# Kernel optimization log

Measured on AMD Instinct MI355X. Metric: run time of the kernel, lower is better.

## Reference

```python
import jax, jax.numpy as jnp
import numpy as np
import math

N_HEAD = 16

def setup_inputs() -> dict:
    key = jax.random.key(0)
    ks = jax.random.split(key, 5)
    B, T, C = 4, 2048, 1024
    x = jax.random.normal(ks[0], (B, T, C), dtype=jnp.float32)
    # xavier-uniform-ish scale for dense kernels
    W_attn = jax.random.normal(ks[1], (C, 3 * C), dtype=jnp.float32) * (1.0 / math.sqrt(C))
    b_attn = jnp.zeros((3 * C,), dtype=jnp.float32)
    W_proj = jax.random.normal(ks[2], (C, C), dtype=jnp.float32) * (1.0 / math.sqrt(C))
    b_proj = jnp.zeros((C,), dtype=jnp.float32)
    return {"x": x, "W_attn": W_attn, "b_attn": b_attn, "W_proj": W_proj, "b_proj": b_proj}

def reference(x, W_attn, b_attn, W_proj, b_proj):
    B, T, C = x.shape
    H = N_HEAD
    D = C // H
    qkv = x @ W_attn + b_attn                      # [B,T,3C]
    q, k, v = jnp.split(qkv, 3, axis=-1)
    q = q.reshape(B, T, H, D).transpose(0, 2, 1, 3)  # [B,H,T,D]
    k = k.reshape(B, T, H, D).transpose(0, 2, 1, 3)
    v = v.reshape(B, T, H, D).transpose(0, 2, 1, 3)
    att = jnp.einsum("bhqd,bhkd->bhqk", q, k) * (1.0 / math.sqrt(D))  # [B,H,T,T]
    causal = jnp.tril(jnp.ones((T, T), dtype=bool))
    att = jnp.where(causal, att, jnp.float32(-jnp.inf))
    att = jax.nn.softmax(att, axis=-1)             # exp(att - logsumexp)
    # dropout rates are 0.0 -> identity
    y = jnp.einsum("bhqk,bhkd->bhqd", att, v)      # [B,H,T,D]
    y = y.transpose(0, 2, 1, 3).reshape(B, T, C)
    y = y @ W_proj + b_proj
    return y
```

## Files before the change

### kernel.cpp

```cpp
#include <hip/hip_runtime.h>
#include <hip/hip_bf16.h>

typedef short s16x8 __attribute__((ext_vector_type(8)));
typedef float f32x4 __attribute__((ext_vector_type(4)));
typedef float f32x2 __attribute__((ext_vector_type(2)));

#define MFMA_BF16(A, B, C) __builtin_amdgcn_mfma_f32_16x16x32_bf16(A, B, C, 0, 0, 0)

constexpr int Bn = 4, Tn = 2048, Cn = 1024, Hn = 16, Dn = 64;
constexpr int Mn = Bn * Tn;
constexpr int Nqkv = 3 * Cn;
constexpr float SC = 0.125f * 1.44269504089f;

__device__ __forceinline__ ushort f2bfu(float f) {
    __hip_bfloat16 h = __float2bfloat16(f);
    return *reinterpret_cast<ushort*>(&h);
}
__device__ __forceinline__ uint pkbf(float a, float b) {
    __hip_bfloat162 h = __float22bfloat162_rn(make_float2(a, b));
    return *reinterpret_cast<uint*>(&h);
}

__device__ __forceinline__ f32x2 pk_add(f32x2 a, f32x2 b) {
    f32x2 d; asm("v_pk_add_f32 %0, %1, %2" : "=v"(d) : "v"(a), "v"(b)); return d;
}
__device__ __forceinline__ f32x2 pk_mul(f32x2 a, f32x2 b) {
    f32x2 d; asm("v_pk_mul_f32 %0, %1, %2" : "=v"(d) : "v"(a), "v"(b)); return d;
}

__device__ __forceinline__ void gl_lds16(const void* g, void* l) {
    __builtin_amdgcn_global_load_lds(
        (const __attribute__((address_space(1))) void*)(uintptr_t)g,
        (__attribute__((address_space(3))) void*)(uint32_t)(uintptr_t)l,
        16, 0, 0);
}

__global__ __launch_bounds__(256) void conv_bf16_kernel(
    const float* __restrict__ src, ushort* __restrict__ dst, int n4)
{
    int i = blockIdx.x * blockDim.x + threadIdx.x;
    int stride = gridDim.x * blockDim.x;
    for (; i < n4; i += stride) {
        float4 v = ((const float4*)src)[i];
        ushort4 o;
        o.x = f2bfu(v.x); o.y = f2bfu(v.y); o.z = f2bfu(v.z); o.w = f2bfu(v.w);
        ((ushort4*)dst)[i] = o;
    }
}

__global__ __launch_bounds__(256) void transpose_cvt_kernel(
    const float* __restrict__ W, ushort* __restrict__ Wt, int K, int N)
{
    __shared__ __align__(16) float Ls[64][68];
    const int t = threadIdx.x;
    const int n0 = blockIdx.x * 64, k0 = blockIdx.y * 64;
#pragma unroll
    for (int p = 0; p < 4; ++p) {
        int r = (t >> 4) + p * 16;
        int c = (t & 15) * 4;
        *(float4*)&Ls[r][c] = *(const float4*)&W[(size_t)(k0 + r) * N + n0 + c];
    }
    __syncthreads();
    const int n = t >> 2;
    const int ks = (t & 3) * 16;
    union { ushort s[16]; uint4 u[2]; } tmp;
#pragma unroll
    for (int j = 0; j < 16; ++j) tmp.s[j] = f2bfu(Ls[ks + j][n]);
    uint4* dp = (uint4*)&Wt[(size_t)(n0 + n) * K + k0 + ks];
    dp[0] = tmp.u[0];
    dp[1] = tmp.u[1];
}

#define GSTAGE(s, b)                                                          \
    _Pragma("unroll")                                                         \
    for (int t_ = 0; t_ < 4; ++t_) {                                          \
        gl_lds16(gA + (size_t)t_ * 8 * Cn + (s) * 64,                         \
                 &As[b][(w * 32 + t_ * 8) * 64]);                             \
        gl_lds16(gB + (size_t)t_ * 8 * Cn + (s) * 64,                         \
                 &Bs[b][(w * 32 + t_ * 8) * 64]);                             \
    }

__global__ __launch_bounds__(256, 2) void qkv_gemm_mfma(
    const ushort* __restrict__ A, const ushort* __restrict__ Bt,
    const float* __restrict__ bias,
    ushort* __restrict__ Qo, ushort* __restrict__ Ko, ushort* __restrict__ Vo)
{
    __shared__ __align__(16) ushort As[2][128 * 64];
    __shared__ __align__(16) ushort Bs[2][128 * 64];
    const int tid = threadIdx.x;
    const int m0 = blockIdx.x * 128, n0 = blockIdx.y * 128;
    const int w = tid >> 6, lane = tid & 63, l15 = lane & 15, qd = lane >> 4;
    const int wm = (w >> 1) * 64, wn = (w & 1) * 64;
    const int lrow = lane >> 3;
    const int lchunk = (lane & 7) ^ (lrow & 7);

    const ushort* gA = A + (size_t)(m0 + w * 32 + lrow) * Cn + lchunk * 8;
    const ushort* gB = Bt + (size_t)(n0 + w * 32 + lrow) * Cn + lchunk * 8;

    f32x4 acc[4][4] = {};
    const bool isV = (n0 >= 2 * Cn);

    GSTAGE(0, 0);
    GSTAGE(1, 1);

    for (int s = 0; s < 16; ++s) {
        if (s < 15) { asm volatile("s_waitcnt vmcnt(8)" ::: "memory"); }
        else        { asm volatile("s_waitcnt vmcnt(0)" ::: "memory"); }
        __builtin_amdgcn_sched_barrier(0);
        __builtin_amdgcn_s_barrier();
        __builtin_amdgcn_sched_barrier(0);

        const ushort* a_ = As[s & 1];
        const ushort* b_ = Bs[s & 1];
        __builtin_amdgcn_s_setprio(1);
#pragma unroll
        for (int ks = 0; ks < 2; ++ks) {
            const int xs = (((ks * 4 + qd) ^ (l15 & 7))) * 8;
            s16x8 af[4], bfr[4];
#pragma unroll
            for (int i = 0; i < 4; ++i) {
                af[i]  = *(const s16x8*)&a_[(wm + i * 16 + l15) * 64 + xs];
                bfr[i] = *(const s16x8*)&b_[(wn + i * 16 + l15) * 64 + xs];
            }
            if (!isV) {
#pragma unroll
                for (int mt = 0; mt < 4; ++mt)
#pragma unroll
                    for (int nt = 0; nt < 4; ++nt)
                        acc[mt][nt] = MFMA_BF16(af[mt], bfr[nt], acc[mt][nt]);
            } else {
#pragma unroll
                for (int mt = 0; mt < 4; ++mt)
#pragma unroll
                    for (int nt = 0; nt < 4; ++nt)
                        acc[nt][mt] = MFMA_BF16(bfr[nt], af[mt], acc[nt][mt]);
            }
        }
        __builtin_amdgcn_s_setprio(0);

        __builtin_amdgcn_sched_barrier(0);
        __builtin_amdgcn_s_barrier();
        __builtin_amdgcn_sched_barrier(0);
        if (s + 2 < 16) { GSTAGE(s + 2, s & 1); }
    }

    if (!isV) {
        const int sel = n0 >> 10;
        ushort* O = (sel == 0) ? Qo : Ko;
        const float scl = (sel == 0) ? SC : 1.0f;
#pragma unroll
        for (int nt = 0; nt < 4; ++nt) {
            const int n_g = n0 + wn + nt * 16 + l15;
            const float bv = bias[n_g];
            const int h = (n_g >> 6) & 15;
            const int d = n_g & 63;
#pragma unroll
            for (int mt = 0; mt < 4; ++mt) {
#pragma unroll
                for (int r = 0; r < 4; ++r) {
                    const int m_g = m0 + wm + mt * 16 + qd * 4 + r;
                    const int b = m_g >> 11, t = m_g & 2047;
                    O[(((size_t)(b * Hn + h) * Tn + t) << 6) + d] =
                        f2bfu((acc[mt][nt][r] + bv) * scl);
                }
            }
        }
    } else {
#pragma unroll
        for (int nt = 0; nt < 4; ++nt) {
            const int n_b = n0 + wn + nt * 16 + qd * 4;
            const float4 bv = *(const float4*)&bias[n_b];
            const int h = (n_b >> 6) & 15;
            const int d0 = n_b & 63;
#pragma unroll
            for (int mt = 0; mt < 4; ++mt) {
                const int m_g = m0 + wm + mt * 16 + l15;
                const int b = m_g >> 11, tt = m_g & 2047;
                const size_t rowb = (size_t)(b * Hn + h) * Dn;
                Vo[(rowb + d0 + 0) * Tn + tt] = f2bfu(acc[nt][mt][0] + bv.x);
                Vo[(rowb + d0 + 1) * Tn + tt] = f2bfu(acc[nt][mt][1] + bv.y);
                Vo[(rowb + d0 + 2) * Tn + tt] = f2bfu(acc[nt][mt][2] + bv.z);
                Vo[(rowb + d0 + 3) * Tn + tt] = f2bfu(acc[nt][mt][3] + bv.w);
            }
        }
    }
}

__global__ __launch_bounds__(256, 4) void attn_mfma(
    const ushort* __restrict__ Q, const ushort* __restrict__ K,
    const ushort* __restrict__ Vt, ushort* __restrict__ Y)
{
    __shared__ __align__(16) ushort Ks[2][64 * 64];
    __shared__ __align__(16) ushort Vs[2][64 * 64];
    __shared__ __align__(16) ushort Ps[64 * 64];

    const int tid = threadIdx.x;
    const int bh = blockIdx.x, bx = blockIdx.y;
    const int w = tid >> 6, lane = tid & 63, l15 = lane & 15, qd = lane >> 4;
    const size_t base = (size_t)bh * Tn * Dn;
    const int lrow = lane >> 3;
    const int lchunk = (lane & 7) ^ (lrow & 7);
    const int q_l = w * 16 + l15;
    const int frow = q_l * 64;
    const int fx0 = ((0 * 4 + qd) ^ (l15 & 7)) * 8;
    const int fx1 = ((1 * 4 + qd) ^ (l15 & 7)) * 8;
    const int b = bh >> 4, h = bh & 15;

    const ushort* Kg = K + base + (size_t)(w * 16 + lrow) * Dn + lchunk * 8;
    const ushort* Vg = Vt + base + (size_t)(w * 16 + lrow) * Tn + lchunk * 8;
    const ushort* Qp = Q + base + (size_t)l15 * Dn + qd * 8;

#pragma unroll
    for (int half = 0; half < 2; ++half) {
        const int qt = half ? (31 - bx) : bx;

        const ushort* qrow = Qp + (size_t)(qt * 64 + w * 16) * Dn;
        s16x8 qf0 = *(const s16x8*)(qrow);
        s16x8 qf1 = *(const s16x8*)(qrow + 32);

        __syncthreads();
#pragma unroll
        for (int t = 0; t < 2; ++t) {
            gl_lds16(Kg + (size_t)(t * 8) * Dn, &Ks[0][(w * 16 + t * 8) * 64]);
            gl_lds16(Vg + (size_t)(t * 8) * Tn, &Vs[0][(w * 16 + t * 8) * 64]);
        }

        float m_run = -1e30f, l_run = 0.f;
        f32x4 o[4] = {};

        for (int kt = 0; kt <= qt; ++kt) {
            const int buf = kt & 1;
            __syncthreads();
            if (kt < qt) {
#pragma unroll
                for (int t = 0; t < 2; ++t) {
                    gl_lds16(Kg + (size_t)((kt + 1) * 64 + t * 8) * Dn,
                             &Ks[buf ^ 1][(w * 16 + t * 8) * 64]);
                    gl_lds16(Vg + (size_t)(t * 8) * Tn + (kt + 1) * 64,
                             &Vs[buf ^ 1][(w * 16 + t * 8) * 64]);
                }
            }

            f32x4 s[4] = {};
            __builtin_amdgcn_s_setprio(1);
#pragma unroll
            for (int nt = 0; nt < 4; ++nt) {
                s16x8 kf = *(const s16x8*)&Ks[buf][(nt * 16 + l15) * 64 + fx0];
                s[nt] = MFMA_BF16(kf, qf0, s[nt]);
            }
#pragma unroll
            for (int nt = 0; nt < 4; ++nt) {
                s16x8 kf = *(const s16x8*)&Ks[buf][(nt * 16 + l15) * 64 + fx1];
                s[nt] = MFMA_BF16(kf, qf1, s[nt]);
            }
            __builtin_amdgcn_s_setprio(0);

            if (kt == qt) {
#pragma unroll
                for (int nt = 0; nt < 4; ++nt)
#pragma unroll
                    for (int r = 0; r < 4; ++r)
                        if (nt * 16 + qd * 4 + r > q_l) s[nt][r] = -1e30f;
            }

            float a0 = fmaxf(fmaxf(s[0][0], s[0][1]), fmaxf(s[0][2], s[0][3]));
            float a1 = fmaxf(fmaxf(s[1][0], s[1][1]), fmaxf(s[1][2], s[1][3]));
            float a2 = fmaxf(fmaxf(s[2][0], s[2][1]), fmaxf(s[2][2], s[2][3]));
            float a3 = fmaxf(fmaxf(s[3][0], s[3][1]), fmaxf(s[3][2], s[3][3]));
            float mx = fmaxf(fmaxf(a0, a1), fmaxf(a2, a3));
            mx = fmaxf(mx, __shfl_xor(mx, 16));
            mx = fmaxf(mx, __shfl_xor(mx, 32));

            if (!__all(mx <= m_run + 8.f)) {
                float m_new = fmaxf(m_run, mx);
                float alpha = exp2f(m_run - m_new);
                m_run = m_new;
                l_run *= alpha;
                f32x2 aa = {alpha, alpha};
#pragma unroll
                for (int dt = 0; dt < 4; ++dt) {
                    o[dt].lo = pk_mul(o[dt].lo, aa);
                    o[dt].hi = pk_mul(o[dt].hi, aa);
                }
            }

            const f32x2 negm = {-m_run, -m_run};
            f32x2 lac0 = {0.f, 0.f}, lac1 = {0.f, 0.f};
#pragma unroll
            for (int nt = 0; nt < 4; ++nt) {
                s[nt].lo = pk_add(s[nt].lo, negm);
                s[nt].hi = pk_add(s[nt].hi, negm);
                s[nt][0] = exp2f(s[nt][0]);
                s[nt][1] = exp2f(s[nt][1]);
                s[nt][2] = exp2f(s[nt][2]);
                s[nt][3] = exp2f(s[nt][3]);
                lac0 = pk_add(lac0, s[nt].lo);
                lac1 = pk_add(lac1, s[nt].hi);
            }
            lac0 = pk_add(lac0, lac1);
            l_run += lac0[0] + lac0[1];

#pragma unroll
            for (int nt = 0; nt < 4; ++nt) {
                uint2 pk;
                pk.x = pkbf(s[nt][0], s[nt][1]);
                pk.y = pkbf(s[nt][2], s[nt][3]);
                const int pc = 2 * nt + (qd >> 1), po = (qd & 1) * 4;
                *(uint2*)&Ps[frow + ((pc ^ (l15 & 7)) * 8) + po] = pk;
            }

            {
                s16x8 pb = *(const s16x8*)&Ps[frow + fx0];
                __builtin_amdgcn_s_setprio(1);
#pragma unroll
                for (int dt = 0; dt < 4; ++dt) {
                    s16x8 vf = *(const s16x8*)&Vs[buf][(dt * 16 + l15) * 64 + fx0];
                    o[dt] = MFMA_BF16(vf, pb, o[dt]);
                }
                pb = *(const s16x8*)&Ps[frow + fx1];
#pragma unroll
                for (int dt = 0; dt < 4; ++dt) {
                    s16x8 vf = *(const s16x8*)&Vs[buf][(dt * 16 + l15) * 64 + fx1];
                    o[dt] = MFMA_BF16(vf, pb, o[dt]);
                }
                __builtin_amdgcn_s_setprio(0);
            }
        }

        float lt = l_run;
        lt += __shfl_xor(lt, 16);
        lt += __shfl_xor(lt, 32);
        const float inv = 1.f / lt;
        const int t_g = qt * 64 + w * 16 + l15;
        ushort* yp = Y + ((size_t)(b * Tn + t_g)) * Cn + h * Dn + qd * 4;
#pragma unroll
        for (int dt = 0; dt < 4; ++dt) {
            uint2 pk;
            pk.x = pkbf(o[dt][0] * inv, o[dt][1] * inv);
            pk.y = pkbf(o[dt][2] * inv, o[dt][3] * inv);
            *(uint2*)(yp + dt * 16) = pk;
        }
    }
}

__global__ __launch_bounds__(256, 2) void proj_gemm_mfma(
    const ushort* __restrict__ A, const ushort* __restrict__ Bt,
    const float* __restrict__ bias, float* __restrict__ out)
{
    __shared__ __align__(16) ushort As[2][128 * 64];
    __shared__ __align__(16) ushort Bs[2][128 * 64];
    const int tid = threadIdx.x;
    const int m0 = blockIdx.x * 128, n0 = blockIdx.y * 128;
    const int w = tid >> 6, lane = tid & 63, l15 = lane & 15, qd = lane >> 4;
    const int wm = (w >> 1) * 64, wn = (w & 1) * 64;
    const int lrow = lane >> 3;
    const int lchunk = (lane & 7) ^ (lrow & 7);

    const ushort* gA = A + (size_t)(m0 + w * 32 + lrow) * Cn + lchunk * 8;
    const ushort* gB = Bt + (size_t)(n0 + w * 32 + lrow) * Cn + lchunk * 8;

    f32x4 acc[4][4] = {};

    GSTAGE(0, 0);
    GSTAGE(1, 1);

    for (int s = 0; s < 16; ++s) {
        if (s < 15) { asm volatile("s_waitcnt vmcnt(8)" ::: "memory"); }
        else        { asm volatile("s_waitcnt vmcnt(0)" ::: "memory"); }
        __builtin_amdgcn_sched_barrier(0);
        __builtin_amdgcn_s_barrier();
        __builtin_amdgcn_sched_barrier(0);

        const ushort* a_ = As[s & 1];
        const ushort* b_ = Bs[s & 1];
        __builtin_amdgcn_s_setprio(1);
#pragma unroll
        for (int ks = 0; ks < 2; ++ks) {
            const int xs = (((ks * 4 + qd) ^ (l15 & 7))) * 8;
            s16x8 af[4], bfr[4];
#pragma unroll
            for (int i = 0; i < 4; ++i) {
                af[i]  = *(const s16x8*)&a_[(wm + i * 16 + l15) * 64 + xs];
                bfr[i] = *(const s16x8*)&b_[(wn + i * 16 + l15) * 64 + xs];
            }
#pragma unroll
            for (int mt = 0; mt < 4; ++mt)
#pragma unroll
                for (int nt = 0; nt < 4; ++nt)
                    acc[mt][nt] = MFMA_BF16(af[mt], bfr[nt], acc[mt][nt]);
        }
        __builtin_amdgcn_s_setprio(0);

        __builtin_amdgcn_sched_barrier(0);
        __builtin_amdgcn_s_barrier();
        __builtin_amdgcn_sched_barrier(0);
        if (s + 2 < 16) { GSTAGE(s + 2, s & 1); }
    }

#pragma unroll
    for (int nt = 0; nt < 4; ++nt) {
        int n_g = n0 + wn + nt * 16 + l15;
        float bv = bias[n_g];
#pragma unroll
        for (int mt = 0; mt < 4; ++mt) {
#pragma unroll
            for (int r = 0; r < 4; ++r) {
                int m_g = m0 + wm + mt * 16 + qd * 4 + r;
                out[(size_t)m_g * Cn + n_g] = acc[mt][nt][r] + bv;
            }
        }
    }
}

extern "C" void kernel_launch(void* const* d_in, const int* in_sizes, int n_in,
                              void* d_out, int out_size, void* d_ws, size_t ws_size,
                              hipStream_t stream) {
    const float* x      = (const float*)d_in[0];
    const float* W_attn = (const float*)d_in[1];
    const float* b_attn = (const float*)d_in[2];
    const float* W_proj = (const float*)d_in[3];
    const float* b_proj = (const float*)d_in[4];
    float* out = (float*)d_out;

    constexpr size_t PER = (size_t)Mn * Cn;
    ushort* Qb  = (ushort*)d_ws;
    ushort* Kb  = Qb + PER;
    ushort* Vtb = Kb + PER;
    ushort* Yb  = Vtb + PER;

    ushort* WtA  = (ushort*)d_out;
    ushort* x_bf = WtA + (size_t)Nqkv * Cn;
    ushort* WtP  = Qb;

    conv_bf16_kernel<<<1024, 256, 0, stream>>>(x, x_bf, (int)(PER / 4));
    transpose_cvt_kernel<<<dim3(Nqkv / 64, Cn / 64), 256, 0, stream>>>(
        W_attn, WtA, Cn, Nqkv);
    qkv_gemm_mfma<<<dim3(Mn / 128, Nqkv / 128), 256, 0, stream>>>(
        x_bf, WtA, b_attn, Qb, Kb, Vtb);
    attn_mfma<<<dim3(Bn * Hn, 16), 256, 0, stream>>>(Qb, Kb, Vtb, Yb);
    transpose_cvt_kernel<<<dim3(Cn / 64, Cn / 64), 256, 0, stream>>>(
        W_proj, WtP, Cn, Cn);
    proj_gemm_mfma<<<dim3(Mn / 128, Cn / 128), 256, 0, stream>>>(
        Yb, WtP, b_proj, out);
}
```

Baseline: 245.8 us.

## Enlarge QKV GEMM tile to 256x256 with 512-thread blocks

The QKV projection GEMM moves from 128x128 tiles with 4 waves to 256x256 tiles with 8 waves. Each wave now computes a 128x64 sub-tile with 8x4 accumulators, and a 1D grid is row-major over m-blocks. The aim is to raise arithmetic intensity and cut global/LDS traffic per FLOP. In exchange, the kernel uses 128KB of LDS per block and more accumulator registers, which can reduce occupancy. The grid also shrinks to 384 blocks, which may leave CUs unevenly loaded.

```diff
diff --git a/kernel.cpp b/kernel.cpp
--- a/kernel.cpp
+++ b/kernel.cpp
@@ -71,7 +71,31 @@
     dp[1] = tmp.u[1];
 }
 
-#define GSTAGE(s, b)                                                          \
+__global__ __launch_bounds__(512, 2) void qkv_gemm_mfma(
+    const ushort* __restrict__ A, const ushort* __restrict__ Bt,
+    const float* __restrict__ bias,
+    ushort* __restrict__ Qo, ushort* __restrict__ Ko, ushort* __restrict__ Vo)
+{
+    __shared__ __align__(16) ushort As[2][256 * 64];
+    __shared__ __align__(16) ushort Bs[2][256 * 64];
+    const int tid = threadIdx.x;
+    const int bid = blockIdx.x;
+    const int mblk = bid / 12, nblk = bid % 12;
+    const int m0 = mblk * 256, n0 = nblk * 256;
+    const int w = tid >> 6;
+    const int lane = tid & 63, l15 = lane & 15, qd = lane >> 4;
+    const int wm = (w >> 2) * 128;
+    const int wn = (w & 3) * 64;
+    const int lrow = lane >> 3;
+    const int lchunk = (lane & 7) ^ (lrow & 7);
+
+    const ushort* gA = A + (size_t)(m0 + w * 32 + lrow) * Cn + lchunk * 8;
+    const ushort* gB = Bt + (size_t)(n0 + w * 32 + lrow) * Cn + lchunk * 8;
+
+    f32x4 acc[8][4] = {};
+    const bool isV = (n0 >= 2 * Cn);
+
+#define QSTAGE(s, b)                                                          \
     _Pragma("unroll")                                                         \
     for (int t_ = 0; t_ < 4; ++t_) {                                          \
         gl_lds16(gA + (size_t)t_ * 8 * Cn + (s) * 64,                         \
@@ -80,28 +104,8 @@
                  &Bs[b][(w * 32 + t_ * 8) * 64]);                             \
     }
 
-__global__ __launch_bounds__(256, 2) void qkv_gemm_mfma(
-    const ushort* __restrict__ A, const ushort* __restrict__ Bt,
-    const float* __restrict__ bias,
-    ushort* __restrict__ Qo, ushort* __restrict__ Ko, ushort* __restrict__ Vo)
-{
-    __shared__ __align__(16) ushort As[2][128 * 64];
-    __shared__ __align__(16) ushort Bs[2][128 * 64];
-    const int tid = threadIdx.x;
-    const int m0 = blockIdx.x * 128, n0 = blockIdx.y * 128;
-    const int w = tid >> 6, lane = tid & 63, l15 = lane & 15, qd = lane >> 4;
-    const int wm = (w >> 1) * 64, wn = (w & 1) * 64;
-    const int lrow = lane >> 3;
-    const int lchunk = (lane & 7) ^ (lrow & 7);
-
-    const ushort* gA = A + (size_t)(m0 + w * 32 + lrow) * Cn + lchunk * 8;
-    const ushort* gB = Bt + (size_t)(n0 + w * 32 + lrow) * Cn + lchunk * 8;
-
-    f32x4 acc[4][4] = {};
-    const bool isV = (n0 >= 2 * Cn);
-
-    GSTAGE(0, 0);
-    GSTAGE(1, 1);
+    QSTAGE(0, 0);
+    QSTAGE(1, 1);
 
     for (int s = 0; s < 16; ++s) {
         if (s < 15) { asm volatile("s_waitcnt vmcnt(8)" ::: "memory"); }
@@ -116,24 +120,25 @@
 #pragma unroll
         for (int ks = 0; ks < 2; ++ks) {
             const int xs = (((ks * 4 + qd) ^ (l15 & 7))) * 8;
-            s16x8 af[4], bfr[4];
-#pragma unroll
-            for (int i = 0; i < 4; ++i) {
-                af[i]  = *(const s16x8*)&a_[(wm + i * 16 + l15) * 64 + xs];
+            s16x8 af[8], bfr[4];
+#pragma unroll
+            for (int i = 0; i < 8; ++i)
+                af[i] = *(const s16x8*)&a_[(wm + i * 16 + l15) * 64 + xs];
+#pragma unroll
+            for (int i = 0; i < 4; ++i)
                 bfr[i] = *(const s16x8*)&b_[(wn + i * 16 + l15) * 64 + xs];
-            }
             if (!isV) {
 #pragma unroll
-                for (int mt = 0; mt < 4; ++mt)
+                for (int mt = 0; mt < 8; ++mt)
 #pragma unroll
                     for (int nt = 0; nt < 4; ++nt)
                         acc[mt][nt] = MFMA_BF16(af[mt], bfr[nt], acc[mt][nt]);
             } else {
 #pragma unroll
-                for (int mt = 0; mt < 4; ++mt)
+                for (int mt = 0; mt < 8; ++mt)
 #pragma unroll
                     for (int nt = 0; nt < 4; ++nt)
-                        acc[nt][mt] = MFMA_BF16(bfr[nt], af[mt], acc[nt][mt]);
+                        acc[mt][nt] = MFMA_BF16(bfr[nt], af[mt], acc[mt][nt]);
             }
         }
         __builtin_amdgcn_s_setprio(0);
@@ -141,8 +146,9 @@
         __builtin_amdgcn_sched_barrier(0);
         __builtin_amdgcn_s_barrier();
         __builtin_amdgcn_sched_barrier(0);
-        if (s + 2 < 16) { GSTAGE(s + 2, s & 1); }
-    }
+        if (s + 2 < 16) { QSTAGE(s + 2, s & 1); }
+    }
+#undef QSTAGE
 
     if (!isV) {
         const int sel = n0 >> 10;
@@ -155,7 +161,7 @@
             const int h = (n_g >> 6) & 15;
             const int d = n_g & 63;
 #pragma unroll
-            for (int mt = 0; mt < 4; ++mt) {
+            for (int mt = 0; mt < 8; ++mt) {
 #pragma unroll
                 for (int r = 0; r < 4; ++r) {
                     const int m_g = m0 + wm + mt * 16 + qd * 4 + r;
@@ -173,14 +179,14 @@
             const int h = (n_b >> 6) & 15;
             const int d0 = n_b & 63;
 #pragma unroll
-            for (int mt = 0; mt < 4; ++mt) {
+            for (int mt = 0; mt < 8; ++mt) {
                 const int m_g = m0 + wm + mt * 16 + l15;
                 const int b = m_g >> 11, tt = m_g & 2047;
                 const size_t rowb = (size_t)(b * Hn + h) * Dn;
-                Vo[(rowb + d0 + 0) * Tn + tt] = f2bfu(acc[nt][mt][0] + bv.x);
-                Vo[(rowb + d0 + 1) * Tn + tt] = f2bfu(acc[nt][mt][1] + bv.y);
-                Vo[(rowb + d0 + 2) * Tn + tt] = f2bfu(acc[nt][mt][2] + bv.z);
-                Vo[(rowb + d0 + 3) * Tn + tt] = f2bfu(acc[nt][mt][3] + bv.w);
+                Vo[(rowb + d0 + 0) * Tn + tt] = f2bfu(acc[mt][nt][0] + bv.x);
+                Vo[(rowb + d0 + 1) * Tn + tt] = f2bfu(acc[mt][nt][1] + bv.y);
+                Vo[(rowb + d0 + 2) * Tn + tt] = f2bfu(acc[mt][nt][2] + bv.z);
+                Vo[(rowb + d0 + 3) * Tn + tt] = f2bfu(acc[mt][nt][3] + bv.w);
             }
         }
     }
@@ -342,6 +348,15 @@
         }
     }
 }
+
+#define GSTAGE(s, b)                                                          \
+    _Pragma("unroll")                                                         \
+    for (int t_ = 0; t_ < 4; ++t_) {                                          \
+        gl_lds16(gA + (size_t)t_ * 8 * Cn + (s) * 64,                         \
+                 &As[b][(w * 32 + t_ * 8) * 64]);                             \
+        gl_lds16(gB + (size_t)t_ * 8 * Cn + (s) * 64,                         \
+                 &Bs[b][(w * 32 + t_ * 8) * 64]);                             \
+    }
 
 __global__ __launch_bounds__(256, 2) void proj_gemm_mfma(
     const ushort* __restrict__ A, const ushort* __restrict__ Bt,
@@ -435,7 +450,7 @@
     conv_bf16_kernel<<<1024, 256, 0, stream>>>(x, x_bf, (int)(PER / 4));
     transpose_cvt_kernel<<<dim3(Nqkv / 64, Cn / 64), 256, 0, stream>>>(
         W_attn, WtA, Cn, Nqkv);
-    qkv_gemm_mfma<<<dim3(Mn / 128, Nqkv / 128), 256, 0, stream>>>(
+    qkv_gemm_mfma<<<(Mn / 256) * (Nqkv / 256), 512, 0, stream>>>(
         x_bf, WtA, b_attn, Qb, Kb, Vtb);
     attn_mfma<<<dim3(Bn * Hn, 16), 256, 0, stream>>>(Qb, Kb, Vtb, Yb);
     transpose_cvt_kernel<<<dim3(Cn / 64, Cn / 64), 256, 0, stream>>>(
```

After: 503.3 us. +104.8%, slower.

## Process 128-query tiles per block with 8 waves sharing K/V tiles

Applied to the files above, without the earlier changes.

The attention kernel now uses 512-thread blocks covering 128 query rows, so each staged K/V tile in shared memory serves twice as many queries. Half the waves load K and the other half load V, and the causal mask is generalized with a key offset across the two diagonal key tiles. This reduces global/LDS staging traffic per query but halves the grid and adds more diagonal work per block, which may hurt occupancy or load balance.

```diff
diff --git a/kernel.cpp b/kernel.cpp
--- a/kernel.cpp
+++ b/kernel.cpp
@@ -186,16 +186,16 @@
     }
 }
 
-__global__ __launch_bounds__(256, 4) void attn_mfma(
+__global__ __launch_bounds__(512, 2) void attn_mfma(
     const ushort* __restrict__ Q, const ushort* __restrict__ K,
     const ushort* __restrict__ Vt, ushort* __restrict__ Y)
 {
     __shared__ __align__(16) ushort Ks[2][64 * 64];
     __shared__ __align__(16) ushort Vs[2][64 * 64];
-    __shared__ __align__(16) ushort Ps[64 * 64];
+    __shared__ __align__(16) ushort Ps[128 * 64];
 
     const int tid = threadIdx.x;
-    const int bh = blockIdx.x, bx = blockIdx.y;
+    const int bh = blockIdx.x, y = blockIdx.y;
     const int w = tid >> 6, lane = tid & 63, l15 = lane & 15, qd = lane >> 4;
     const size_t base = (size_t)bh * Tn * Dn;
     const int lrow = lane >> 3;
@@ -205,39 +205,48 @@
     const int fx0 = ((0 * 4 + qd) ^ (l15 & 7)) * 8;
     const int fx1 = ((1 * 4 + qd) ^ (l15 & 7)) * 8;
     const int b = bh >> 4, h = bh & 15;
-
-    const ushort* Kg = K + base + (size_t)(w * 16 + lrow) * Dn + lchunk * 8;
-    const ushort* Vg = Vt + base + (size_t)(w * 16 + lrow) * Tn + lchunk * 8;
+    const int w3 = w & 3;
+    const bool stageK = (w < 4);
+
+    const ushort* Kg = K + base + (size_t)(w3 * 16 + lrow) * Dn + lchunk * 8;
+    const ushort* Vg = Vt + base + (size_t)(w3 * 16 + lrow) * Tn + lchunk * 8;
     const ushort* Qp = Q + base + (size_t)l15 * Dn + qd * 8;
 
 #pragma unroll
     for (int half = 0; half < 2; ++half) {
-        const int qt = half ? (31 - bx) : bx;
-
-        const ushort* qrow = Qp + (size_t)(qt * 64 + w * 16) * Dn;
+        const int qt = half ? (15 - y) : y;
+        const int ktend = 2 * qt + 1;
+
+        const ushort* qrow = Qp + (size_t)(qt * 128 + w * 16) * Dn;
         s16x8 qf0 = *(const s16x8*)(qrow);
         s16x8 qf1 = *(const s16x8*)(qrow + 32);
 
         __syncthreads();
-#pragma unroll
-        for (int t = 0; t < 2; ++t) {
-            gl_lds16(Kg + (size_t)(t * 8) * Dn, &Ks[0][(w * 16 + t * 8) * 64]);
-            gl_lds16(Vg + (size_t)(t * 8) * Tn, &Vs[0][(w * 16 + t * 8) * 64]);
+        if (stageK) {
+            gl_lds16(Kg, &Ks[0][(w3 * 16) * 64]);
+            gl_lds16(Kg + (size_t)8 * Dn, &Ks[0][(w3 * 16 + 8) * 64]);
+        } else {
+            gl_lds16(Vg, &Vs[0][(w3 * 16) * 64]);
+            gl_lds16(Vg + (size_t)8 * Tn, &Vs[0][(w3 * 16 + 8) * 64]);
         }
 
         float m_run = -1e30f, l_run = 0.f;
         f32x4 o[4] = {};
 
-        for (int kt = 0; kt <= qt; ++kt) {
+        for (int kt = 0; kt <= ktend; ++kt) {
             const int buf = kt & 1;
             __syncthreads();
-            if (kt < qt) {
-#pragma unroll
-                for (int t = 0; t < 2; ++t) {
-                    gl_lds16(Kg + (size_t)((kt + 1) * 64 + t * 8) * Dn,
-                             &Ks[buf ^ 1][(w * 16 + t * 8) * 64]);
-                    gl_lds16(Vg + (size_t)(t * 8) * Tn + (kt + 1) * 64,
-                             &Vs[buf ^ 1][(w * 16 + t * 8) * 64]);
+            if (kt < ktend) {
+                if (stageK) {
+                    gl_lds16(Kg + (size_t)((kt + 1) * 64) * Dn,
+                             &Ks[buf ^ 1][(w3 * 16) * 64]);
+                    gl_lds16(Kg + (size_t)((kt + 1) * 64 + 8) * Dn,
+                             &Ks[buf ^ 1][(w3 * 16 + 8) * 64]);
+                } else {
+                    gl_lds16(Vg + (size_t)(kt + 1) * 64,
+                             &Vs[buf ^ 1][(w3 * 16) * 64]);
+                    gl_lds16(Vg + (size_t)8 * Tn + (kt + 1) * 64,
+                             &Vs[buf ^ 1][(w3 * 16 + 8) * 64]);
                 }
             }
 
@@ -255,12 +264,14 @@
             }
             __builtin_amdgcn_s_setprio(0);
 
-            if (kt == qt) {
+            const int koff = kt * 64 - qt * 128;
+            if (koff >= 0) {
 #pragma unroll
                 for (int nt = 0; nt < 4; ++nt)
 #pragma unroll
                     for (int r = 0; r < 4; ++r)
-                        if (nt * 16 + qd * 4 + r > q_l) s[nt][r] = -1e30f;
+                        if (koff + nt * 16 + qd * 4 + r > q_l)
+                            s[nt][r] = -1e30f;
             }
 
             float a0 = fmaxf(fmaxf(s[0][0], s[0][1]), fmaxf(s[0][2], s[0][3]));
@@ -331,7 +342,7 @@
         lt += __shfl_xor(lt, 16);
         lt += __shfl_xor(lt, 32);
         const float inv = 1.f / lt;
-        const int t_g = qt * 64 + w * 16 + l15;
+        const int t_g = qt * 128 + q_l;
         ushort* yp = Y + ((size_t)(b * Tn + t_g)) * Cn + h * Dn + qd * 4;
 #pragma unroll
         for (int dt = 0; dt < 4; ++dt) {
@@ -437,7 +448,7 @@
         W_attn, WtA, Cn, Nqkv);
     qkv_gemm_mfma<<<dim3(Mn / 128, Nqkv / 128), 256, 0, stream>>>(
         x_bf, WtA, b_attn, Qb, Kb, Vtb);
-    attn_mfma<<<dim3(Bn * Hn, 16), 256, 0, stream>>>(Qb, Kb, Vtb, Yb);
+    attn_mfma<<<dim3(Bn * Hn, 8), 512, 0, stream>>>(Qb, Kb, Vtb, Yb);
     transpose_cvt_kernel<<<dim3(Cn / 64, Cn / 64), 256, 0, stream>>>(
         W_proj, WtP, Cn, Cn);
     proj_gemm_mfma<<<dim3(Mn / 128, Cn / 128), 256, 0, stream>>>(
```

New measurement: 252.1 us. 1.03x slower.
